# Kernel tuning notes

Hardware: AMD Instinct MI355X
Metric: run time of the kernel (lower is better)

Reference implementation:

```python
import jax, jax.numpy as jnp
import numpy as np

# ----- static layer configuration (mirrors __init__ / _precompute_cg_tensor) -----
NODE_LS = [0, 0, 1, 1]          # node_l_values (multiplicity expressed via repetition; node_multiplicity=1)
EDGE_SH = 1                      # edge_sh_degree
H_LS = NODE_LS + NODE_LS + [0]   # l-values of h = [f_src, f_tgt, d]
H_DIMS = [2 * l + 1 for l in H_LS]
H_OFF = np.concatenate([[0], np.cumsum(H_DIMS)])
A_DIMS = [2 * l + 1 for l in range(EDGE_SH + 1)]
A_OFF = np.concatenate([[0], np.cumsum(A_DIMS)])
O_DIMS = [2 * l + 1 for l in NODE_LS]
O_OFF = np.concatenate([[0], np.cumsum(O_DIMS)])
F_DIM = int(O_OFF[-1])           # 8
A_DIM = int(A_OFF[-1])           # 4
N_NODES, N_EDGES = 100000, 1600000
MLP_DIMS = [2 * len(NODE_LS) + 1, 64, 32, len(NODE_LS)]  # 9 -> 64 -> 32 -> 4

def _levi_civita():
    e = np.zeros((3, 3, 3), np.float32)
    e[0, 1, 2] = e[1, 2, 0] = e[2, 0, 1] = 1.0
    e[0, 2, 1] = e[2, 1, 0] = e[1, 0, 2] = -1.0
    return e

# real SO(3) Clebsch-Gordan tensors (e3nn wigner_3j normalization: full contraction norm 1)
_CG = {
    (0, 0, 0): np.ones((1, 1, 1), np.float32),
    (0, 1, 1): (np.eye(3, dtype=np.float32) / np.sqrt(3.0)).reshape(1, 3, 3),
    (1, 0, 1): (np.eye(3, dtype=np.float32) / np.sqrt(3.0)).reshape(3, 1, 3),
    (1, 1, 0): (np.eye(3, dtype=np.float32) / np.sqrt(3.0)).reshape(3, 3, 1),
    (1, 1, 1): _levi_civita() / np.sqrt(6.0),
}

CONNECTIONS = []  # (h_idx, a_l, out_idx, cg[h,a,o]) -- same enumeration order as the torch loop
for _h_idx, _hl in enumerate(H_LS):
    for _al in range(EDGE_SH + 1):
        for _oi, _ol in enumerate(NODE_LS):
            if abs(_hl - _al) <= _ol <= _hl + _al and (_hl, _al, _ol) in _CG:
                CONNECTIONS.append((_h_idx, _al, _oi, jnp.asarray(_CG[(_hl, _al, _ol)])))


def _invariants(x):
    # s_i = [f_{l=0}, ||f_{l=1}||, ...] per l-slot (multiplicity 1)
    outs = []
    for i, l in enumerate(NODE_LS):
        s, e = int(O_OFF[i]), int(O_OFF[i + 1])
        if l == 0:
            outs.append(x[:, s:e])
        else:
            outs.append(jnp.linalg.norm(x[:, s:e], axis=1, keepdims=True))
    return jnp.concatenate(outs, axis=1)


def setup_inputs() -> dict:
    ks = jax.random.split(jax.random.key(0), 10)
    edge_index = jax.random.randint(ks[0], (2, N_EDGES), 0, N_NODES)
    f = jax.random.normal(ks[1], (N_NODES, F_DIM), jnp.float32)
    d = jax.random.uniform(ks[2], (N_EDGES, 1), jnp.float32)
    a = jax.random.normal(ks[3], (N_EDGES, A_DIM), jnp.float32)
    w1 = jax.random.normal(ks[4], (EDGE_SH + 1,), jnp.float32) * 0.1
    w2 = jax.random.normal(ks[5], (EDGE_SH + 1,), jnp.float32) * 0.1
    W0 = jax.random.normal(ks[6], (MLP_DIMS[0], MLP_DIMS[1]), jnp.float32) / np.sqrt(MLP_DIMS[0])
    b0 = jnp.zeros((MLP_DIMS[1],), jnp.float32)
    W1 = jax.random.normal(ks[7], (MLP_DIMS[1], MLP_DIMS[2]), jnp.float32) / np.sqrt(MLP_DIMS[1])
    b1 = jnp.zeros((MLP_DIMS[2],), jnp.float32)
    W2 = jax.random.normal(ks[8], (MLP_DIMS[2], MLP_DIMS[3]), jnp.float32) / np.sqrt(MLP_DIMS[2])
    b2 = jnp.zeros((MLP_DIMS[3],), jnp.float32)
    return {"edge_index": edge_index, "f": f, "d": d, "a": a, "w1": w1, "w2": w2,
            "W0": W0, "b0": b0, "W1": W1, "b1": b1, "W2": W2, "b2": b2}


def reference(edge_index, f, d, a, w1, w2, W0, b0, W1, b1, W2, b2):
    src, tgt = edge_index[0], edge_index[1]
    n = f.shape[0]
    h = jnp.concatenate([f[src], f[tgt], d], axis=1)  # [E, 17]
    messages = jnp.zeros((h.shape[0], F_DIM), f.dtype)
    for h_idx, a_l, out_idx, cg in CONNECTIONS:
        hs, he = int(H_OFF[h_idx]), int(H_OFF[h_idx + 1])
        as_, ae = int(A_OFF[a_l]), int(A_OFF[a_l + 1])
        os_, oe = int(O_OFF[out_idx]), int(O_OFF[out_idx + 1])
        raw = jnp.einsum('hao,eh,ea->eo', cg, h[:, hs:he], a[:, as_:ae])  # [E, 2*out_l+1]
        msg = jnp.tanh(w2[a_l] * jnp.tanh(w1[a_l] * raw))
        messages = messages.at[:, os_:oe].add(msg)
    agg = jax.ops.segment_sum(messages, tgt, num_segments=n)          # [N, 8]
    dist_sum = jax.ops.segment_sum(d, tgt, num_segments=n)           # [N, 1]
    counts = jax.ops.segment_sum(jnp.ones((h.shape[0],), f.dtype), tgt, num_segments=n)
    avg_d = dist_sum / (counts[:, None] + 1e-8)
    psi_in = jnp.concatenate([_invariants(f), _invariants(agg), avg_d], axis=1)  # [N, 9]
    x = jax.nn.relu(psi_in @ W0 + b0)
    x = jax.nn.relu(x @ W1 + b1)
    gates = jax.nn.sigmoid(x @ W2 + b2)  # [N, 4]
    gate_full = jnp.concatenate(
        [jnp.repeat(gates[:, i:i + 1], O_DIMS[i], axis=1) for i in range(len(NODE_LS))], axis=1)
    return f + gate_full * agg
```

## Files before the change

kernel.cpp:

```cpp
#include <hip/hip_runtime.h>
#include <math.h>

#define IS3 0.57735026918962576f
#define IS6 0.40824829046386302f

#define SHIFT 11
#define BSZ   2048
#define CAP   36864u
#define SEG   6
#define MQ    4096.0f
#define IMQ   (1.0f/4096.0f)

__device__ __forceinline__ float fastrcp(float x) { return __builtin_amdgcn_rcpf(x); }

__device__ __forceinline__ float Tnl(float x, float tw1, float w2) {
    float e = __expf(tw1 * x);
    float u = 1.0f - 2.0f * fastrcp(e + 1.0f);
    float z = w2 * u;
    float z2 = z * z;
    float p = __builtin_fmaf(z2, 0.133333333f, -0.333333333f);
    return __builtin_fmaf(z * z2, p, z);
}

__device__ __forceinline__ int q16(float x) {
    int v = (int)rintf(x * MQ);
    v = v >  32767 ?  32767 : v;
    v = v < -32768 ? -32768 : v;
    return v;
}

__global__ __launch_bounds__(1024, 8) void route_kernel(
    const int* __restrict__ ei, const float* __restrict__ f,
    const float* __restrict__ d, const float* __restrict__ a,
    const float* __restrict__ w1p, const float* __restrict__ w2p,
    unsigned* __restrict__ tails,
    unsigned* __restrict__ qmeta,
    uint2* __restrict__ qmsg,
    int E, int nbuk)
{
    __shared__ unsigned hcnt[64];
    __shared__ unsigned hoff[64];
    int tid = threadIdx.x;
    if (tid < 64) hcnt[tid] = 0;

    int e = blockIdx.x * 1024 + tid;
    bool valid = (e < E);

    float tw10 = 2.0f * w1p[0], tw11 = 2.0f * w1p[1];
    float w20 = w2p[0], w21 = w2p[1];

    int t = 0, s = 0;
    float4 sA = make_float4(0.f,0.f,0.f,0.f), sB = sA, tA = sA, tB = sA, av = sA;
    float de = 0.f;
    if (valid) {
        t = ei[E + e];
        s = ei[e];
        const float4* f4 = (const float4*)f;
        sA = f4[2*s]; sB = f4[2*s+1];
        tA = f4[2*t]; tB = f4[2*t+1];
        de = d[e];
        av = ((const float4*)a)[e];
    }

    __syncthreads();

    unsigned b = 0, lrank = 0;
    if (valid) {
        b = (((unsigned)t) >> SHIFT) & 63u;
        lrank = atomicAdd(&hcnt[b], 1u);
    }
    __syncthreads();

    unsigned basek = 0;
    if (tid < nbuk && hcnt[tid] != 0u)
        basek = atomicAdd(&tails[tid * 64], hcnt[tid]);

    unsigned dq = 0;
    uint2 pk = make_uint2(0u, 0u);
    if (valid) {
        float a0 = av.x, ax = av.y, ay = av.z, az = av.w;

        float sc[5] = { sA.x, sA.y, tA.x, tA.y, de };
        float vx[4] = { sA.z, sB.y, tA.z, tB.y };
        float vy[4] = { sA.w, sB.z, tA.w, tB.z };
        float vz[4] = { sB.x, sB.w, tB.x, tB.w };

        float mS = 0.f, mX = 0.f, mY = 0.f, mZ = 0.f;
        #pragma unroll
        for (int i = 0; i < 5; ++i) {
            mS += Tnl(sc[i] * a0, tw10, w20);
            mX += Tnl(sc[i] * ax * IS3, tw11, w21);
            mY += Tnl(sc[i] * ay * IS3, tw11, w21);
            mZ += Tnl(sc[i] * az * IS3, tw11, w21);
        }
        #pragma unroll
        for (int i = 0; i < 4; ++i) {
            float dva = vx[i]*ax + vy[i]*ay + vz[i]*az;
            mS += Tnl(dva * IS3, tw11, w21);
            mX += Tnl(vx[i] * a0 * IS3, tw10, w20);
            mY += Tnl(vy[i] * a0 * IS3, tw10, w20);
            mZ += Tnl(vz[i] * a0 * IS3, tw10, w20);
            float cx = vy[i]*az - vz[i]*ay;
            float cy = vz[i]*ax - vx[i]*az;
            float cz = vx[i]*ay - vy[i]*ax;
            mX += Tnl(cx * IS6, tw11, w21);
            mY += Tnl(cy * IS6, tw11, w21);
            mZ += Tnl(cz * IS6, tw11, w21);
        }

        unsigned dqi = (unsigned)(de * 2047.0f + 0.5f);
        dq = dqi > 2047u ? 2047u : dqi;
        int qS = q16(mS), qX = q16(mX), qY = q16(mY), qZ = q16(mZ);
        pk.x = ((unsigned)(unsigned short)qS) | (((unsigned)(unsigned short)qX) << 16);
        pk.y = ((unsigned)(unsigned short)qY) | (((unsigned)(unsigned short)qZ) << 16);
    }

    if (tid < nbuk) hoff[tid] = basek;
    __syncthreads();

    if (valid) {
        unsigned pos = hoff[b] + lrank;
        if (pos < CAP) {
            size_t idx = (size_t)b * CAP + pos;
            qmeta[idx] = (((unsigned)(t & (BSZ - 1))) << 11) | dq;
            qmsg[idx]  = pk;
        }
    }
}

__global__ __launch_bounds__(1024) void bucket_kernel(
    const unsigned* __restrict__ tails, const unsigned* __restrict__ qmeta,
    const uint2* __restrict__ qmsg, unsigned* __restrict__ partial, int nbuk)
{
    __shared__ unsigned long long accSX[BSZ];
    __shared__ unsigned long long accYZ[BSZ];
    __shared__ unsigned accM[BSZ];
    int wg = blockIdx.x;
    int b = wg / SEG, sgi = wg % SEG;
    for (int i = threadIdx.x; i < BSZ; i += 1024) {
        accSX[i] = 0ull; accYZ[i] = 0ull; accM[i] = 0u;
    }
    __syncthreads();

    unsigned tail = tails[b * 64];
    if (tail > CAP) tail = CAP;
    unsigned lo = (unsigned)(((unsigned long long)tail * sgi) / SEG);
    unsigned hi = (unsigned)(((unsigned long long)tail * (sgi + 1)) / SEG);
    size_t base = (size_t)b * CAP;

    for (unsigned q = lo + threadIdx.x; q < hi; q += 1024) {
        unsigned meta = qmeta[base + q];
        uint2 m = qmsg[base + q];
        int local = (int)(meta >> 11);
        int qS = (int)(short)(m.x & 0xFFFFu);
        int qX = (int)(short)(m.x >> 16);
        int qY = (int)(short)(m.y & 0xFFFFu);
        int qZ = (int)(short)(m.y >> 16);
        unsigned long long vSX =
            (((unsigned long long)(unsigned)qX) << 32) | (unsigned)(qS + 65536);
        unsigned long long vYZ =
            (((unsigned long long)(unsigned)qZ) << 32) | (unsigned)(qY + 65536);
        atomicAdd(&accSX[local], vSX);
        atomicAdd(&accYZ[local], vYZ);
        atomicAdd(&accM[local], (1u << 20) | (meta & 2047u));
    }
    __syncthreads();

    unsigned* dst = partial + (size_t)wg * (BSZ * 5);
    for (int i = threadIdx.x; i < BSZ; i += 1024) {
        unsigned long long sx = accSX[i], yz = accYZ[i];
        dst[0*BSZ + i] = (unsigned)sx;
        dst[1*BSZ + i] = (unsigned)(sx >> 32);
        dst[2*BSZ + i] = (unsigned)yz;
        dst[3*BSZ + i] = (unsigned)(yz >> 32);
        dst[4*BSZ + i] = accM[i];
    }
}

__global__ __launch_bounds__(256) void mlp_kernel(
    const float* __restrict__ f, const unsigned* __restrict__ partial,
    const float* __restrict__ W0, const float* __restrict__ b0,
    const float* __restrict__ W1, const float* __restrict__ b1,
    const float* __restrict__ W2, const float* __restrict__ b2,
    float* __restrict__ out, int N)
{
    __shared__ float4 sW0t4[64*3];
    __shared__ float4 sW1v[64*8];
    __shared__ float4 sW2v[32];
    __shared__ float  sb0[64];
    __shared__ float4 sb1v[8];
    __shared__ float4 sb2v[1];

    int tid = threadIdx.x;
    float* w0t = (float*)sW0t4;
    for (int idx = tid; idx < 576; idx += 256) {
        int k = idx >> 6, i = idx & 63;
        w0t[i * 12 + k] = W0[idx];
    }
    if (tid < 192) {
        int i = tid / 3, k = 9 + tid % 3;
        w0t[i * 12 + k] = 0.f;
    }
    { float* p = (float*)sW1v; for (int idx = tid; idx < 2048; idx += 256) p[idx] = W1[idx]; }
    { float* p = (float*)sW2v; if (tid < 128) p[tid] = W2[tid]; }
    if (tid < 64) sb0[tid] = b0[tid];
    { float* p = (float*)sb1v; if (tid < 32) p[tid] = b1[tid]; }
    { float* p = (float*)sb2v; if (tid < 4)  p[tid] = b2[tid]; }
    __syncthreads();

    int n = blockIdx.x * 256 + tid;
    if (n >= N) return;

    int b = n >> SHIFT;
    int local = n & (BSZ - 1);
    int S = 0, X = 0, Y = 0, Z = 0, cnt = 0, dqs = 0;
    #pragma unroll
    for (int s2 = 0; s2 < SEG; ++s2) {
        const unsigned* p = partial + ((size_t)(b * SEG + s2)) * (BSZ * 5);
        unsigned m4 = p[4*BSZ + local];
        int c = (int)(m4 >> 20);
        S += (int)p[0*BSZ + local] - (c << 16);
        X += (int)p[1*BSZ + local];
        Y += (int)p[2*BSZ + local] - (c << 16);
        Z += (int)p[3*BSZ + local];
        dqs += (int)(m4 & 0xFFFFFu);
        cnt += c;
    }
    float aS = (float)S * IMQ, ax = (float)X * IMQ;
    float ay = (float)Y * IMQ, az = (float)Z * IMQ;
    float cf = (float)cnt;
    float dsum = (float)dqs * (1.0f / 2047.0f);

    float4 fA = ((const float4*)f)[2*n];
    float4 fB = ((const float4*)f)[2*n+1];

    float nrm1 = sqrtf(fA.z*fA.z + fA.w*fA.w + fB.x*fB.x);
    float nrm2 = sqrtf(fB.y*fB.y + fB.z*fB.z + fB.w*fB.w);
    float nv   = sqrtf(ax*ax + ay*ay + az*az);
    float avgd = dsum * fastrcp(cf + 1e-8f);
    float4 p0 = make_float4(fA.x, fA.y, nrm1, nrm2);
    float4 p1 = make_float4(aS, aS, nv, nv);
    float4 p2 = make_float4(avgd, 0.f, 0.f, 0.f);

    float x1s[32];
    #pragma unroll
    for (int j = 0; j < 8; ++j) {
        float4 bv = sb1v[j];
        x1s[4*j+0] = bv.x; x1s[4*j+1] = bv.y; x1s[4*j+2] = bv.z; x1s[4*j+3] = bv.w;
    }
    #pragma unroll
    for (int i = 0; i < 64; ++i) {
        float4 r0 = sW0t4[i*3+0], r1 = sW0t4[i*3+1], r2 = sW0t4[i*3+2];
        float acc = sb0[i]
            + r0.x*p0.x + r0.y*p0.y + r0.z*p0.z + r0.w*p0.w
            + r1.x*p1.x + r1.y*p1.y + r1.z*p1.z + r1.w*p1.w
            + r2.x*p2.x;
        acc = fmaxf(acc, 0.f);
        #pragma unroll
        for (int j = 0; j < 8; ++j) {
            float4 wv = sW1v[i*8+j];
            x1s[4*j+0] += acc * wv.x;
            x1s[4*j+1] += acc * wv.y;
            x1s[4*j+2] += acc * wv.z;
            x1s[4*j+3] += acc * wv.w;
        }
    }
    #pragma unroll
    for (int j = 0; j < 32; ++j) x1s[j] = fmaxf(x1s[j], 0.f);

    float4 gb = sb2v[0];
    float g0 = gb.x, g1 = gb.y, g2 = gb.z, g3 = gb.w;
    #pragma unroll
    for (int i = 0; i < 32; ++i) {
        float4 wv = sW2v[i];
        g0 += x1s[i] * wv.x;
        g1 += x1s[i] * wv.y;
        g2 += x1s[i] * wv.z;
        g3 += x1s[i] * wv.w;
    }
    g0 = fastrcp(1.0f + __expf(-g0));
    g1 = fastrcp(1.0f + __expf(-g1));
    g2 = fastrcp(1.0f + __expf(-g2));
    g3 = fastrcp(1.0f + __expf(-g3));

    float* o = out + (size_t)8*n;
    o[0] = fA.x + g0*aS;
    o[1] = fA.y + g1*aS;
    o[2] = fA.z + g2*ax;
    o[3] = fA.w + g2*ay;
    o[4] = fB.x + g2*az;
    o[5] = fB.y + g3*ax;
    o[6] = fB.z + g3*ay;
    o[7] = fB.w + g3*az;
}

extern "C" void kernel_launch(void* const* d_in, const int* in_sizes, int n_in,
                              void* d_out, int out_size, void* d_ws, size_t ws_size,
                              hipStream_t stream) {
    const int*   ei = (const int*)d_in[0];
    const float* f  = (const float*)d_in[1];
    const float* d  = (const float*)d_in[2];
    const float* a  = (const float*)d_in[3];
    const float* w1 = (const float*)d_in[4];
    const float* w2 = (const float*)d_in[5];
    const float* W0 = (const float*)d_in[6];
    const float* b0 = (const float*)d_in[7];
    const float* W1 = (const float*)d_in[8];
    const float* b1 = (const float*)d_in[9];
    const float* W2 = (const float*)d_in[10];
    const float* b2 = (const float*)d_in[11];
    int E = in_sizes[0] / 2;
    int N = in_sizes[1] / 8;
    int nbuk = (N + BSZ - 1) >> SHIFT;

    char* w = (char*)d_ws;
    size_t qn = (size_t)nbuk * CAP;
    uint2*    qmsg    = (uint2*)w;
    unsigned* qmeta   = (unsigned*)(w + qn * 8);
    unsigned* partial = (unsigned*)(w + qn * 12);
    unsigned* tails   = (unsigned*)(w + qn * 12
                        + (size_t)nbuk * SEG * BSZ * 5 * 4);

    hipMemsetAsync(tails, 0, (size_t)nbuk * 64 * sizeof(unsigned), stream);

    int EB = (E + 1023) / 1024;
    route_kernel <<<dim3(EB), dim3(1024), 0, stream>>>(
        ei, f, d, a, w1, w2, tails, qmeta, qmsg, E, nbuk);
    bucket_kernel<<<dim3(nbuk * SEG), dim3(1024), 0, stream>>>(
        tails, qmeta, qmsg, partial, nbuk);
    mlp_kernel   <<<dim3((N + 255) / 256), dim3(256), 0, stream>>>(
        f, partial, W0, b0, W1, b1, W2, b2, (float*)d_out, N);
}
```

Measured before the change: 175.4 us.

## Use Pade tanh approximation, size bucket segments from workspace, widen MLP blocks

Replaces the exp-plus-reciprocal inner tanh with a clamped rational (Pade) approximation built from FMAs and one reciprocal. Makes the bucket segment count a runtime value chosen from the free workspace, capped near 512 workgroups, so the per-bucket accumulation spreads over more blocks. Doubles the MLP block size to 512 threads. The Pade form with clamping at 3.5 adds approximation error in the tanh, and the runtime seg count removes the unrolled reduction loop in the MLP kernel.

```diff
diff --git a/kernel.cpp b/kernel.cpp
--- a/kernel.cpp
+++ b/kernel.cpp
@@ -7,19 +7,24 @@
 #define SHIFT 11
 #define BSZ   2048
 #define CAP   36864u
-#define SEG   6
 #define MQ    4096.0f
 #define IMQ   (1.0f/4096.0f)
 
 __device__ __forceinline__ float fastrcp(float x) { return __builtin_amdgcn_rcpf(x); }
 
-__device__ __forceinline__ float Tnl(float x, float tw1, float w2) {
-    float e = __expf(tw1 * x);
-    float u = 1.0f - 2.0f * fastrcp(e + 1.0f);
+__device__ __forceinline__ float Tnl(float x, float w1, float w2) {
+    float y = w1 * x;
+    y = fminf(fmaxf(y, -3.5f), 3.5f);
+    float t = y * y;
+    float p = t + 105.0f;
+    p = __builtin_fmaf(p, t, 945.0f);
+    float q = __builtin_fmaf(15.0f, t, 420.0f);
+    q = __builtin_fmaf(q, t, 945.0f);
+    float u = y * p * fastrcp(q);
     float z = w2 * u;
     float z2 = z * z;
-    float p = __builtin_fmaf(z2, 0.133333333f, -0.333333333f);
-    return __builtin_fmaf(z * z2, p, z);
+    float pp = __builtin_fmaf(z2, 0.133333333f, -0.333333333f);
+    return __builtin_fmaf(z * z2, pp, z);
 }
 
 __device__ __forceinline__ int q16(float x) {
@@ -46,7 +51,7 @@
     int e = blockIdx.x * 1024 + tid;
     bool valid = (e < E);
 
-    float tw10 = 2.0f * w1p[0], tw11 = 2.0f * w1p[1];
+    float w10 = w1p[0], w11 = w1p[1];
     float w20 = w2p[0], w21 = w2p[1];
 
     int t = 0, s = 0;
@@ -88,24 +93,24 @@
         float mS = 0.f, mX = 0.f, mY = 0.f, mZ = 0.f;
         #pragma unroll
         for (int i = 0; i < 5; ++i) {
-            mS += Tnl(sc[i] * a0, tw10, w20);
-            mX += Tnl(sc[i] * ax * IS3, tw11, w21);
-            mY += Tnl(sc[i] * ay * IS3, tw11, w21);
-            mZ += Tnl(sc[i] * az * IS3, tw11, w21);
+            mS += Tnl(sc[i] * a0, w10, w20);
+            mX += Tnl(sc[i] * ax * IS3, w11, w21);
+            mY += Tnl(sc[i] * ay * IS3, w11, w21);
+            mZ += Tnl(sc[i] * az * IS3, w11, w21);
         }
         #pragma unroll
         for (int i = 0; i < 4; ++i) {
             float dva = vx[i]*ax + vy[i]*ay + vz[i]*az;
-            mS += Tnl(dva * IS3, tw11, w21);
-            mX += Tnl(vx[i] * a0 * IS3, tw10, w20);
-            mY += Tnl(vy[i] * a0 * IS3, tw10, w20);
-            mZ += Tnl(vz[i] * a0 * IS3, tw10, w20);
+            mS += Tnl(dva * IS3, w11, w21);
+            mX += Tnl(vx[i] * a0 * IS3, w10, w20);
+            mY += Tnl(vy[i] * a0 * IS3, w10, w20);
+            mZ += Tnl(vz[i] * a0 * IS3, w10, w20);
             float cx = vy[i]*az - vz[i]*ay;
             float cy = vz[i]*ax - vx[i]*az;
             float cz = vx[i]*ay - vy[i]*ax;
-            mX += Tnl(cx * IS6, tw11, w21);
-            mY += Tnl(cy * IS6, tw11, w21);
-            mZ += Tnl(cz * IS6, tw11, w21);
+            mX += Tnl(cx * IS6, w11, w21);
+            mY += Tnl(cy * IS6, w11, w21);
+            mZ += Tnl(cz * IS6, w11, w21);
         }
 
         unsigned dqi = (unsigned)(de * 2047.0f + 0.5f);
@@ -130,13 +135,14 @@
 
 __global__ __launch_bounds__(1024) void bucket_kernel(
     const unsigned* __restrict__ tails, const unsigned* __restrict__ qmeta,
-    const uint2* __restrict__ qmsg, unsigned* __restrict__ partial, int nbuk)
+    const uint2* __restrict__ qmsg, unsigned* __restrict__ partial,
+    int nbuk, int seg)
 {
     __shared__ unsigned long long accSX[BSZ];
     __shared__ unsigned long long accYZ[BSZ];
     __shared__ unsigned accM[BSZ];
     int wg = blockIdx.x;
-    int b = wg / SEG, sgi = wg % SEG;
+    int b = wg / seg, sgi = wg % seg;
     for (int i = threadIdx.x; i < BSZ; i += 1024) {
         accSX[i] = 0ull; accYZ[i] = 0ull; accM[i] = 0u;
     }
@@ -144,8 +150,8 @@
 
     unsigned tail = tails[b * 64];
     if (tail > CAP) tail = CAP;
-    unsigned lo = (unsigned)(((unsigned long long)tail * sgi) / SEG);
-    unsigned hi = (unsigned)(((unsigned long long)tail * (sgi + 1)) / SEG);
+    unsigned lo = (unsigned)(((unsigned long long)tail * sgi) / seg);
+    unsigned hi = (unsigned)(((unsigned long long)tail * (sgi + 1)) / seg);
     size_t base = (size_t)b * CAP;
 
     for (unsigned q = lo + threadIdx.x; q < hi; q += 1024) {
@@ -177,12 +183,12 @@
     }
 }
 
-__global__ __launch_bounds__(256) void mlp_kernel(
+__global__ __launch_bounds__(512) void mlp_kernel(
     const float* __restrict__ f, const unsigned* __restrict__ partial,
     const float* __restrict__ W0, const float* __restrict__ b0,
     const float* __restrict__ W1, const float* __restrict__ b1,
     const float* __restrict__ W2, const float* __restrict__ b2,
-    float* __restrict__ out, int N)
+    float* __restrict__ out, int N, int seg)
 {
     __shared__ float4 sW0t4[64*3];
     __shared__ float4 sW1v[64*8];
@@ -193,7 +199,7 @@
 
     int tid = threadIdx.x;
     float* w0t = (float*)sW0t4;
-    for (int idx = tid; idx < 576; idx += 256) {
+    for (int idx = tid; idx < 576; idx += 512) {
         int k = idx >> 6, i = idx & 63;
         w0t[i * 12 + k] = W0[idx];
     }
@@ -201,22 +207,21 @@
         int i = tid / 3, k = 9 + tid % 3;
         w0t[i * 12 + k] = 0.f;
     }
-    { float* p = (float*)sW1v; for (int idx = tid; idx < 2048; idx += 256) p[idx] = W1[idx]; }
+    { float* p = (float*)sW1v; for (int idx = tid; idx < 2048; idx += 512) p[idx] = W1[idx]; }
     { float* p = (float*)sW2v; if (tid < 128) p[tid] = W2[tid]; }
     if (tid < 64) sb0[tid] = b0[tid];
     { float* p = (float*)sb1v; if (tid < 32) p[tid] = b1[tid]; }
     { float* p = (float*)sb2v; if (tid < 4)  p[tid] = b2[tid]; }
     __syncthreads();
 
-    int n = blockIdx.x * 256 + tid;
+    int n = blockIdx.x * 512 + tid;
     if (n >= N) return;
 
     int b = n >> SHIFT;
     int local = n & (BSZ - 1);
     int S = 0, X = 0, Y = 0, Z = 0, cnt = 0, dqs = 0;
-    #pragma unroll
-    for (int s2 = 0; s2 < SEG; ++s2) {
-        const unsigned* p = partial + ((size_t)(b * SEG + s2)) * (BSZ * 5);
+    for (int s2 = 0; s2 < seg; ++s2) {
+        const unsigned* p = partial + ((size_t)(b * seg + s2)) * (BSZ * 5);
         unsigned m4 = p[4*BSZ + local];
         int c = (int)(m4 >> 20);
         S += (int)p[0*BSZ + local] - (c << 16);
@@ -313,21 +318,31 @@
     int N = in_sizes[1] / 8;
     int nbuk = (N + BSZ - 1) >> SHIFT;
 
+    size_t qn = (size_t)nbuk * CAP;
+    size_t fixed = qn * 12 + (size_t)nbuk * 64 * 4;
+    size_t per_seg = (size_t)nbuk * BSZ * 5 * 4;
+    int segmax = nbuk > 0 ? (512 / nbuk) : 6;
+    if (segmax < 1) segmax = 1;
+    int seg = 6;
+    if (ws_size > fixed + per_seg) {
+        size_t m = (ws_size - fixed) / per_seg;
+        seg = (int)(m < (size_t)segmax ? m : (size_t)segmax);
+        if (seg < 1) seg = 1;
+    }
+
     char* w = (char*)d_ws;
-    size_t qn = (size_t)nbuk * CAP;
     uint2*    qmsg    = (uint2*)w;
     unsigned* qmeta   = (unsigned*)(w + qn * 8);
     unsigned* partial = (unsigned*)(w + qn * 12);
-    unsigned* tails   = (unsigned*)(w + qn * 12
-                        + (size_t)nbuk * SEG * BSZ * 5 * 4);
+    unsigned* tails   = (unsigned*)(w + qn * 12 + (size_t)seg * per_seg);
 
     hipMemsetAsync(tails, 0, (size_t)nbuk * 64 * sizeof(unsigned), stream);
 
     int EB = (E + 1023) / 1024;
     route_kernel <<<dim3(EB), dim3(1024), 0, stream>>>(
         ei, f, d, a, w1, w2, tails, qmeta, qmsg, E, nbuk);
-    bucket_kernel<<<dim3(nbuk * SEG), dim3(1024), 0, stream>>>(
-        tails, qmeta, qmsg, partial, nbuk);
-    mlp_kernel   <<<dim3((N + 255) / 256), dim3(256), 0, stream>>>(
-        f, partial, W0, b0, W1, b1, W2, b2, (float*)d_out, N);
-}
+    bucket_kernel<<<dim3(nbuk * seg), dim3(1024), 0, stream>>>(
+        tails, qmeta, qmsg, partial, nbuk, seg);
+    mlp_kernel   <<<dim3((N + 511) / 512), dim3(512), 0, stream>>>(
+        f, partial, W0, b0, W1, b1, W2, b2, (float*)d_out, N, seg);
+}
```

After: 181.8 us. 3.6% more time.
